# Kernel tuning notes

Hardware: AMD Instinct MI355X
Metric: run time of the kernel (lower is better)

## Reference

```python
import jax, jax.numpy as jnp
import numpy as np
import math

L, Bt, ED, H, LU = 1024, 64, 512, 512, 60
PSSM_DIM = 21

def setup_inputs() -> dict:
    key = jax.random.key(0)
    ks = jax.random.split(key, 16)
    seq = jax.random.randint(ks[0], (L, Bt), 0, 20)
    pssm = jax.random.uniform(ks[1], (L, Bt, PSSM_DIM), dtype=jnp.float32)
    length = jnp.full((Bt,), L, dtype=jnp.int32)  # all full-length -> packing is identity
    embed = jax.random.normal(ks[2], (20, ED), dtype=jnp.float32)
    s = 1.0 / math.sqrt(H)
    def u(k, shape):
        return jax.random.uniform(k, shape, minval=-s, maxval=s, dtype=jnp.float32)
    Wih_f = u(ks[3], (4 * H, ED + PSSM_DIM)); Whh_f = u(ks[4], (4 * H, H))
    bih_f = u(ks[5], (4 * H,)); bhh_f = u(ks[6], (4 * H,))
    Wih_b = u(ks[7], (4 * H, ED + PSSM_DIM)); Whh_b = u(ks[8], (4 * H, H))
    bih_b = u(ks[9], (4 * H,)); bhh_b = u(ks[10], (4 * H,))
    sl = 1.0 / math.sqrt(2 * H)
    W_lin = jax.random.uniform(ks[11], (LU, 2 * H), minval=-sl, maxval=sl, dtype=jnp.float32)
    b_lin = jax.random.uniform(ks[12], (LU,), minval=-sl, maxval=sl, dtype=jnp.float32)
    alphabet = jax.random.uniform(ks[13], (LU, 3), minval=-math.pi, maxval=math.pi, dtype=jnp.float32)
    return dict(seq=seq, pssm=pssm, length=length, embed=embed,
                Wih_f=Wih_f, Whh_f=Whh_f, bih_f=bih_f, bhh_f=bhh_f,
                Wih_b=Wih_b, Whh_b=Whh_b, bih_b=bih_b, bhh_b=bhh_b,
                W_lin=W_lin, b_lin=b_lin, alphabet=alphabet)

def _lstm_dir(x, Wih, Whh, bih, bhh, reverse):
    # x: [L, B, D] -> hidden states [L, B, H]
    b = bih + bhh
    xg = jnp.einsum('lbd,gd->lbg', x, Wih) + b  # precompute input gates
    B = x.shape[1]
    Hh = Whh.shape[1]
    def step(carry, xgt):
        h, c = carry
        z = xgt + h @ Whh.T
        i, f, g, o = jnp.split(z, 4, axis=-1)  # torch gate order i,f,g,o
        i = jax.nn.sigmoid(i); f = jax.nn.sigmoid(f)
        g = jnp.tanh(g); o = jax.nn.sigmoid(o)
        c = f * c + i * g
        h = o * jnp.tanh(c)
        return (h, c), h
    init = (jnp.zeros((B, Hh), x.dtype), jnp.zeros((B, Hh), x.dtype))
    _, hs = jax.lax.scan(step, init, xg, reverse=reverse)
    return hs

def _extend(A, B, C, R, T, P):
    # NeRF extension: A,B,C [Bt,3]; R,T scalars; P [Bt] torsion
    D2 = jnp.stack([-R * jnp.cos(T) * jnp.ones_like(P),
                    R * jnp.cos(P) * jnp.sin(T),
                    R * jnp.sin(P) * jnp.sin(T)], axis=1)  # [Bt,3]
    bc = C - B
    bc = bc / jnp.linalg.norm(bc, axis=1, keepdims=True)
    n = jnp.cross(B - A, bc)
    n = n / jnp.linalg.norm(n, axis=1, keepdims=True)
    M = jnp.stack([bc, jnp.cross(n, bc), n], axis=2)  # [Bt,3,3]
    return jnp.einsum('bij,bj->bi', M, D2) + C

def reference(seq, pssm, length, embed, Wih_f, Whh_f, bih_f, bhh_f,
              Wih_b, Whh_b, bih_b, bhh_b, W_lin, b_lin, alphabet):
    bond_lengths = jnp.array([132.868, 145.801, 152.326], dtype=pssm.dtype)
    bond_angles = jnp.array([2.028, 2.124, 1.941], dtype=pssm.dtype)
    x = jnp.concatenate([embed[seq], pssm], axis=2)  # [L,B,ED+21]
    h_f = _lstm_dir(x, Wih_f, Whh_f, bih_f, bhh_f, reverse=False)
    h_b = _lstm_dir(x, Wih_b, Whh_b, bih_b, bhh_b, reverse=True)
    lstm_out = jnp.concatenate([h_f, h_b], axis=2)  # [L,B,2H]
    logits = jnp.einsum('lbh,uh->lbu', lstm_out, W_lin) + b_lin
    p = jax.nn.softmax(logits, axis=2)  # [L,B,LU]
    sin = p @ jnp.sin(alphabet)  # [L,B,3]
    cos = p @ jnp.cos(alphabet)
    phi = jnp.arctan2(sin, cos)  # [L,B,3] torsion angles
    B_ = seq.shape[1]
    init_coords = jnp.broadcast_to(jnp.eye(3, dtype=pssm.dtype)[:, None, :], (3, B_, 3))
    def residue_step(carry, phi_i):
        A, Bp, C = carry
        outs = []
        for j in range(3):  # N, CA, C backbone atoms
            D = _extend(A, Bp, C, bond_lengths[j], bond_angles[j], phi_i[:, j])
            A, Bp, C = Bp, C, D
            outs.append(D)
        return (A, Bp, C), jnp.stack(outs)  # [3,Bt,3]
    carry0 = (init_coords[0], init_coords[1], init_coords[2])
    _, new = jax.lax.scan(residue_step, carry0, phi)  # [L,3,Bt,3]
    coords = jnp.concatenate([init_coords, new.reshape(-1, B_, 3)], axis=0)  # [3+3L,B,3]
    return coords
```

## Files before the change

### kernel.cpp

```cpp
#include <hip/hip_runtime.h>
#include <hip/hip_bf16.h>
#include <hip/hip_fp16.h>
#include <math.h>

constexpr int L    = 1024;
constexpr int B    = 64;
constexpr int H    = 512;
constexpr int ED   = 512;
constexpr int PSSM = 21;
constexpr int DIN  = ED + PSSM;
constexpr int LU   = 60;
constexpr int HB   = H * B;
constexpr int NWG_DIR = 32;
constexpr int UPW  = 16;

typedef __attribute__((ext_vector_type(8))) _Float16 half8;
typedef __attribute__((ext_vector_type(4))) float f32x4;

__global__ __launch_bounds__(256) void prep_e2(
    const float* __restrict__ Wih_f, const float* __restrict__ Wih_b,
    const float* __restrict__ bih_f, const float* __restrict__ bhh_f,
    const float* __restrict__ bih_b, const float* __restrict__ bhh_b,
    const float* __restrict__ embed, float* __restrict__ E2)
{
    int idx  = blockIdx.x * 256 + threadIdx.x;
    int col  = idx & 2047;
    int rest = idx >> 11;
    int s    = rest % 20;
    int dir  = rest / 20;
    const float* W  = dir ? Wih_b : Wih_f;
    const float* er = embed + (size_t)s * ED;
    const float* wr = W + (size_t)col * DIN;
    float a = 0.f;
    #pragma unroll 8
    for (int k = 0; k < ED; ++k) a = fmaf(er[k], wr[k], a);
    a += (dir ? bih_b : bih_f)[col] + (dir ? bhh_b : bhh_f)[col];
    E2[idx] = a;
}

__global__ __launch_bounds__(256) void prep_whh(
    const float* __restrict__ Whh_f, const float* __restrict__ Whh_b,
    unsigned short* __restrict__ hi, unsigned short* __restrict__ lo)
{
    int idx = blockIdx.x * 256 + threadIdx.x;
    const int NPD = 2048 * 512;
    float w = (idx < NPD) ? Whh_f[idx] : Whh_b[idx - NPD];
    __half h = __float2half_rn(w);
    __half l2 = __float2half_rn(w - __half2float(h));
    hi[idx] = __half_as_ushort(h);
    lo[idx] = __half_as_ushort(l2);
}

__global__ __launch_bounds__(256, 1) void lstm_mfma(
    const float* __restrict__ E2, const float* __restrict__ pssm,
    const int* __restrict__ seq,
    const float* __restrict__ Wih_f, const float* __restrict__ Wih_b,
    const unsigned short* __restrict__ WhhHi, const unsigned short* __restrict__ WhhLo,
    unsigned short* __restrict__ ring,
    unsigned short* __restrict__ hs16_f, unsigned short* __restrict__ hs16_b,
    int* __restrict__ cnt)
{
    __shared__ unsigned short bhi[4 * 16 * 64 * 8];
    __shared__ unsigned short blo[4 * 16 * 64 * 8];
    __shared__ float wpsh[4][PSSM][16];
    __shared__ float wesh[20][68];
    __shared__ unsigned short tbuf[4][16][20];

    const int wg    = blockIdx.x;
    const int dir   = wg >> 5;
    const int wslot = wg & 31;
    const int j0    = wslot * UPW;
    const int tid   = threadIdx.x;
    const int l     = tid & 63;
    const int q     = tid >> 6;
    const int u     = l & 15;
    const int kh    = l >> 4;
    const int m0    = q * 16 + kh * 4;

    const float* Wih = dir ? Wih_b : Wih_f;
    const float* E2d = E2 + (size_t)dir * 20 * 2048;
    const unsigned short* Whi = WhhHi + (size_t)dir * 2048 * 512;
    const unsigned short* Wlo = WhhLo + (size_t)dir * 2048 * 512;
    unsigned short* rbase = ring + (size_t)dir * 2 * HB;
    unsigned short* hist  = dir ? hs16_b : hs16_f;
    int* qflg = cnt + ((size_t)(dir * 4 + q)) * L;

    for (int i = tid; i < 4 * 16 * 64; i += 256) {
        int l2 = i & 63, c2 = (i >> 6) & 15, g2 = i >> 10;
        int row = g2 * 512 + j0 + (l2 & 15);
        size_t off = (size_t)row * 512 + c2 * 32 + (l2 >> 4) * 8;
        *(uint4*)&bhi[i * 8] = *(const uint4*)(Whi + off);
        *(uint4*)&blo[i * 8] = *(const uint4*)(Wlo + off);
    }
    for (int i = tid; i < 4 * PSSM * 16; i += 256) {
        int uu = i & 15, rem = i >> 4;
        int k = rem % PSSM, g = rem / PSSM;
        wpsh[g][k][uu] = Wih[(size_t)(g * 512 + j0 + uu) * DIN + ED + k];
    }
    for (int i = tid; i < 20 * 64; i += 256) {
        int sym = i >> 6, col = i & 63;
        wesh[sym][col] = E2d[(size_t)sym * 2048 + (col >> 4) * 512 + j0 + (col & 15)];
    }
    __syncthreads();

    float creg[4] = {0.f, 0.f, 0.f, 0.f};

    for (int s = 0; s < L; ++s) {
        const int t = dir ? (L - 1 - s) : s;

        float zin[4][4];
        int sb[4];
        #pragma unroll
        for (int r = 0; r < 4; ++r) sb[r] = seq[t * B + m0 + r];
        #pragma unroll
        for (int g = 0; g < 4; ++g)
            #pragma unroll
            for (int r = 0; r < 4; ++r)
                zin[g][r] = wesh[sb[r]][g * 16 + u];
        {
            const float* pb = pssm + (size_t)t * B * PSSM;
            #pragma unroll
            for (int k = 0; k < PSSM; ++k) {
                float p0 = pb[(m0 + 0) * PSSM + k];
                float p1 = pb[(m0 + 1) * PSSM + k];
                float p2 = pb[(m0 + 2) * PSSM + k];
                float p3 = pb[(m0 + 3) * PSSM + k];
                #pragma unroll
                for (int g = 0; g < 4; ++g) {
                    float wv = wpsh[g][k][u];
                    zin[g][0] = fmaf(p0, wv, zin[g][0]);
                    zin[g][1] = fmaf(p1, wv, zin[g][1]);
                    zin[g][2] = fmaf(p2, wv, zin[g][2]);
                    zin[g][3] = fmaf(p3, wv, zin[g][3]);
                }
            }
        }

        f32x4 acc[4];
        #pragma unroll
        for (int g = 0; g < 4; ++g)
            acc[g] = (f32x4){zin[g][0], zin[g][1], zin[g][2], zin[g][3]};

        if (s > 0) {
            {
                const int* fp = qflg + (s - 1);
                int it = 0;
                while (true) {
                    int v;
                    asm volatile("global_load_dword %0, %1, off sc0 sc1\n\t"
                                 "s_waitcnt vmcnt(0)"
                                 : "=v"(v) : "v"(fp) : "memory");
                    if (__all(v >= NWG_DIR)) break;
                    __builtin_amdgcn_s_sleep(1);
                    if (++it > (1 << 17)) break;
                }
            }
            uint4 af[16];
            const unsigned short* src =
                rbase + ((s + 1) & 1) * HB + (size_t)(q * 16 + u) * 512 + kh * 8;
            #pragma unroll
            for (int c = 0; c < 16; ++c)
                asm volatile("global_load_dwordx4 %0, %1, off sc0 sc1"
                             : "=&v"(af[c]) : "v"(src + c * 32) : "memory");
            asm volatile("s_waitcnt vmcnt(0)" ::: "memory");
            __builtin_amdgcn_sched_barrier(0);

            #pragma unroll
            for (int c = 0; c < 16; ++c) {
                half8 ah = *(const half8*)&af[c];
                #pragma unroll
                for (int g = 0; g < 4; ++g) {
                    half8 bh = *(const half8*)&bhi[((g * 16 + c) * 64 + l) * 8];
                    half8 bl = *(const half8*)&blo[((g * 16 + c) * 64 + l) * 8];
                    acc[g] = __builtin_amdgcn_mfma_f32_16x16x32_f16(ah, bh, acc[g], 0, 0, 0);
                    acc[g] = __builtin_amdgcn_mfma_f32_16x16x32_f16(ah, bl, acc[g], 0, 0, 0);
                }
            }
        }

        #pragma unroll
        for (int r = 0; r < 4; ++r) {
            float iv = acc[0][r], fv = acc[1][r], gv = acc[2][r], ov = acc[3][r];
            iv = 1.f / (1.f + __expf(-iv));
            fv = 1.f / (1.f + __expf(-fv));
            gv = tanhf(gv);
            ov = 1.f / (1.f + __expf(-ov));
            float cc = fv * creg[r] + iv * gv;
            creg[r] = cc;
            float hv = ov * tanhf(cc);
            tbuf[q][kh * 4 + r][u] = __half_as_ushort(__float2half_rn(hv));
        }

        {
            int bq = l >> 2, g4 = (l & 3) * 4;
            int bb = q * 16 + bq;
            unsigned v0 = *(const unsigned*)&tbuf[q][bq][g4];
            unsigned v1 = *(const unsigned*)&tbuf[q][bq][g4 + 2];
            unsigned short* d = rbase + (s & 1) * HB + bb * 512 + j0 + g4;
            asm volatile("global_store_dword %0, %1, off sc0 sc1"
                         :: "v"(d), "v"(v0) : "memory");
            asm volatile("global_store_dword %0, %1, off sc0 sc1"
                         :: "v"(d + 2), "v"(v1) : "memory");
            unsigned short* hd = hist + (size_t)t * HB + bb * 512 + j0 + g4;
            *(unsigned*)hd = v0;
            *(unsigned*)(hd + 2) = v1;
        }
        asm volatile("s_waitcnt vmcnt(0)" ::: "memory");
        if (l == 0) atomicAdd(qflg + s, 1);
    }
}

__global__ __launch_bounds__(256) void proj_softmax(
    const unsigned short* __restrict__ hsf, const unsigned short* __restrict__ hsb,
    const float* __restrict__ W_lin, const float* __restrict__ b_lin,
    const float* __restrict__ alphabet, float* __restrict__ sp, float* __restrict__ cp)
{
    const int t   = blockIdx.x;
    const int tid = threadIdx.x;
    const int b   = tid & 63;
    const int ug  = __builtin_amdgcn_readfirstlane(tid >> 6);
    constexpr int NU = 15;

    __shared__ float lg[B][LU];
    __shared__ float sa[LU][3], ca[LU][3];
    if (tid < LU) {
        for (int k = 0; k < 3; ++k) {
            float a = alphabet[tid * 3 + k];
            sa[tid][k] = __sinf(a);
            ca[tid][k] = __cosf(a);
        }
    }

    const int u0 = ug * NU;
    float acc[NU];
    #pragma unroll
    for (int i = 0; i < NU; ++i) acc[i] = b_lin[u0 + i];

    #pragma unroll
    for (int half = 0; half < 2; ++half) {
        const unsigned short* hp =
            (half ? hsb : hsf) + (size_t)t * HB + (size_t)b * H;
        for (int j8 = 0; j8 < H / 8; ++j8) {
            uint4 hv4 = *(const uint4*)(hp + j8 * 8);
            const __half* hx = (const __half*)&hv4;
            float hvv[8];
            #pragma unroll
            for (int jj = 0; jj < 8; ++jj) hvv[jj] = __half2float(hx[jj]);
            #pragma unroll
            for (int i = 0; i < NU; ++i) {
                const float* wr = W_lin + (size_t)(u0 + i) * (2 * H) + half * H + j8 * 8;
                float4 wa = *(const float4*)wr;
                float4 wb = *(const float4*)(wr + 4);
                acc[i] = fmaf(hvv[0], wa.x, acc[i]);
                acc[i] = fmaf(hvv[1], wa.y, acc[i]);
                acc[i] = fmaf(hvv[2], wa.z, acc[i]);
                acc[i] = fmaf(hvv[3], wa.w, acc[i]);
                acc[i] = fmaf(hvv[4], wb.x, acc[i]);
                acc[i] = fmaf(hvv[5], wb.y, acc[i]);
                acc[i] = fmaf(hvv[6], wb.z, acc[i]);
                acc[i] = fmaf(hvv[7], wb.w, acc[i]);
            }
        }
    }
    #pragma unroll
    for (int i = 0; i < NU; ++i) lg[b][u0 + i] = acc[i];
    __syncthreads();

    if (tid < B) {
        float m = -1e30f;
        for (int u = 0; u < LU; ++u) m = fmaxf(m, lg[tid][u]);
        float sv[3] = {0, 0, 0}, cv[3] = {0, 0, 0};
        for (int u = 0; u < LU; ++u) {
            float e = __expf(lg[tid][u] - m);
            for (int k = 0; k < 3; ++k) {
                sv[k] = fmaf(e, sa[u][k], sv[k]);
                cv[k] = fmaf(e, ca[u][k], cv[k]);
            }
        }
        for (int k = 0; k < 3; ++k) {
            float r = rsqrtf(sv[k] * sv[k] + cv[k] * cv[k]);
            sp[((size_t)t * B + tid) * 3 + k] = sv[k] * r;
            cp[((size_t)t * B + tid) * 3 + k] = cv[k] * r;
        }
    }
}

__global__ void geometry(const float* __restrict__ sp, const float* __restrict__ cp,
                         float* __restrict__ out)
{
    const int b = threadIdx.x;
    const float Rj[3] = {132.868f, 145.801f, 152.326f};
    const float Tj[3] = {2.028f, 2.124f, 1.941f};
    float cT[3], sT[3];
    for (int j = 0; j < 3; ++j) { cT[j] = cosf(Tj[j]); sT[j] = sinf(Tj[j]); }

    for (int r = 0; r < 3; ++r)
        for (int c = 0; c < 3; ++c)
            out[((size_t)r * B + b) * 3 + c] = (r == c) ? 1.f : 0.f;

    float Ax = 1.f, Ay = 0.f, Az = 0.f;
    float Bx = 0.f, By = 1.f, Bz = 0.f;
    float Cx = 0.f, Cy = 0.f, Cz = 1.f;

    for (int t = 0; t < L; ++t) {
        for (int j = 0; j < 3; ++j) {
            float sP = sp[((size_t)t * B + b) * 3 + j];
            float cP = cp[((size_t)t * B + b) * 3 + j];
            float d0 = -Rj[j] * cT[j];
            float d1 =  Rj[j] * cP * sT[j];
            float d2 =  Rj[j] * sP * sT[j];

            float bcx = Cx - Bx, bcy = Cy - By, bcz = Cz - Bz;
            float inv = rsqrtf(bcx * bcx + bcy * bcy + bcz * bcz);
            bcx *= inv; bcy *= inv; bcz *= inv;

            float abx = Bx - Ax, aby = By - Ay, abz = Bz - Az;
            float nx = aby * bcz - abz * bcy;
            float ny = abz * bcx - abx * bcz;
            float nz = abx * bcy - aby * bcx;
            inv = rsqrtf(nx * nx + ny * ny + nz * nz);
            nx *= inv; ny *= inv; nz *= inv;

            float mx = ny * bcz - nz * bcy;
            float my = nz * bcx - nx * bcz;
            float mz = nx * bcy - ny * bcx;

            float Dx = bcx * d0 + mx * d1 + nx * d2 + Cx;
            float Dy = bcy * d0 + my * d1 + ny * d2 + Cy;
            float Dz = bcz * d0 + mz * d1 + nz * d2 + Cz;

            size_t r = 3 + 3 * (size_t)t + j;
            out[(r * B + b) * 3 + 0] = Dx;
            out[(r * B + b) * 3 + 1] = Dy;
            out[(r * B + b) * 3 + 2] = Dz;

            Ax = Bx; Ay = By; Az = Bz;
            Bx = Cx; By = Cy; Bz = Cz;
            Cx = Dx; Cy = Dy; Cz = Dz;
        }
    }
}

extern "C" void kernel_launch(void* const* d_in, const int* in_sizes, int n_in,
                              void* d_out, int out_size, void* d_ws, size_t ws_size,
                              hipStream_t stream)
{
    const int*   seq      = (const int*)  d_in[0];
    const float* pssm     = (const float*)d_in[1];
    const float* embed    = (const float*)d_in[3];
    const float* Wih_f    = (const float*)d_in[4];
    const float* Whh_f    = (const float*)d_in[5];
    const float* bih_f    = (const float*)d_in[6];
    const float* bhh_f    = (const float*)d_in[7];
    const float* Wih_b    = (const float*)d_in[8];
    const float* Whh_b    = (const float*)d_in[9];
    const float* bih_b    = (const float*)d_in[10];
    const float* bhh_b    = (const float*)d_in[11];
    const float* W_lin    = (const float*)d_in[12];
    const float* b_lin    = (const float*)d_in[13];
    const float* alphabet = (const float*)d_in[14];
    float* out = (float*)d_out;

    char* ws = (char*)d_ws;
    unsigned short* ring = (unsigned short*)ws;
    int* cnt       = (int*)(ws + 262144);
    float* E2      = (float*)(ws + 294912);
    unsigned short* WhhHi = (unsigned short*)(ws + 622592);
    unsigned short* WhhLo = (unsigned short*)(ws + 622592 + 4194304);
    unsigned short* hs16_f = (unsigned short*)(ws + 622592 + 8388608);
    unsigned short* hs16_b = (unsigned short*)(ws + 622592 + 8388608 + 67108864);
    float* sp      = (float*)(ws + 294912);
    float* cp      = (float*)(ws + 294912 + 786432);

    (void)hipMemsetAsync(cnt, 0, 32768, stream);

    prep_e2<<<dim3(320), dim3(256), 0, stream>>>(Wih_f, Wih_b, bih_f, bhh_f,
                                                 bih_b, bhh_b, embed, E2);
    prep_whh<<<dim3(8192), dim3(256), 0, stream>>>(Whh_f, Whh_b, WhhHi, WhhLo);

    lstm_mfma<<<dim3(2 * NWG_DIR), dim3(256), 0, stream>>>(
        E2, pssm, seq, Wih_f, Wih_b, WhhHi, WhhLo,
        ring, hs16_f, hs16_b, cnt);

    proj_softmax<<<dim3(L), dim3(256), 0, stream>>>(
        hs16_f, hs16_b, W_lin, b_lin, alphabet, sp, cp);
    geometry<<<dim3(1), dim3(64), 0, stream>>>(sp, cp, out);
}
```

Measured before the change: 7.603 ms.

## Replace counter-flag barrier with sentinel-poisoned history buffer polling

```diff
diff --git a/kernel.cpp b/kernel.cpp
--- a/kernel.cpp
+++ b/kernel.cpp
@@ -56,9 +56,7 @@
     const int* __restrict__ seq,
     const float* __restrict__ Wih_f, const float* __restrict__ Wih_b,
     const unsigned short* __restrict__ WhhHi, const unsigned short* __restrict__ WhhLo,
-    unsigned short* __restrict__ ring,
-    unsigned short* __restrict__ hs16_f, unsigned short* __restrict__ hs16_b,
-    int* __restrict__ cnt)
+    unsigned short* __restrict__ hs16_f, unsigned short* __restrict__ hs16_b)
 {
     __shared__ unsigned short bhi[4 * 16 * 64 * 8];
     __shared__ unsigned short blo[4 * 16 * 64 * 8];
@@ -81,9 +79,7 @@
     const float* E2d = E2 + (size_t)dir * 20 * 2048;
     const unsigned short* Whi = WhhHi + (size_t)dir * 2048 * 512;
     const unsigned short* Wlo = WhhLo + (size_t)dir * 2048 * 512;
-    unsigned short* rbase = ring + (size_t)dir * 2 * HB;
     unsigned short* hist  = dir ? hs16_b : hs16_f;
-    int* qflg = cnt + ((size_t)(dir * 4 + q)) * L;
 
     for (int i = tid; i < 4 * 16 * 64; i += 256) {
         int l2 = i & 63, c2 = (i >> 6) & 15, g2 = i >> 10;
@@ -106,7 +102,8 @@
     float creg[4] = {0.f, 0.f, 0.f, 0.f};
 
     for (int s = 0; s < L; ++s) {
-        const int t = dir ? (L - 1 - s) : s;
+        const int t     = dir ? (L - 1 - s) : s;
+        const int tprev = dir ? (t + 1) : (t - 1);
 
         float zin[4][4];
         int sb[4];
@@ -142,27 +139,29 @@
             acc[g] = (f32x4){zin[g][0], zin[g][1], zin[g][2], zin[g][3]};
 
         if (s > 0) {
-            {
-                const int* fp = qflg + (s - 1);
-                int it = 0;
-                while (true) {
-                    int v;
-                    asm volatile("global_load_dword %0, %1, off sc0 sc1\n\t"
-                                 "s_waitcnt vmcnt(0)"
-                                 : "=v"(v) : "v"(fp) : "memory");
-                    if (__all(v >= NWG_DIR)) break;
-                    __builtin_amdgcn_s_sleep(1);
-                    if (++it > (1 << 17)) break;
-                }
-            }
             uint4 af[16];
             const unsigned short* src =
-                rbase + ((s + 1) & 1) * HB + (size_t)(q * 16 + u) * 512 + kh * 8;
-            #pragma unroll
-            for (int c = 0; c < 16; ++c)
-                asm volatile("global_load_dwordx4 %0, %1, off sc0 sc1"
-                             : "=&v"(af[c]) : "v"(src + c * 32) : "memory");
-            asm volatile("s_waitcnt vmcnt(0)" ::: "memory");
+                hist + (size_t)tprev * HB + (size_t)(q * 16 + u) * 512 + kh * 8;
+            int it = 0;
+            while (true) {
+                #pragma unroll
+                for (int c = 0; c < 16; ++c)
+                    asm volatile("global_load_dwordx4 %0, %1, off sc0 sc1"
+                                 : "=&v"(af[c]) : "v"(src + c * 32) : "memory");
+                asm volatile("s_waitcnt vmcnt(0)" ::: "memory");
+                __builtin_amdgcn_sched_barrier(0);
+                unsigned bad = 0u;
+                #pragma unroll
+                for (int c = 0; c < 16; ++c) {
+                    bad |= (unsigned)(af[c].x == 0xFFFFFFFFu);
+                    bad |= (unsigned)(af[c].y == 0xFFFFFFFFu);
+                    bad |= (unsigned)(af[c].z == 0xFFFFFFFFu);
+                    bad |= (unsigned)(af[c].w == 0xFFFFFFFFu);
+                }
+                if (__all(bad == 0u)) break;
+                __builtin_amdgcn_s_sleep(1);
+                if (++it > (1 << 17)) break;
+            }
             __builtin_amdgcn_sched_barrier(0);
 
             #pragma unroll
@@ -196,17 +195,12 @@
             int bb = q * 16 + bq;
             unsigned v0 = *(const unsigned*)&tbuf[q][bq][g4];
             unsigned v1 = *(const unsigned*)&tbuf[q][bq][g4 + 2];
-            unsigned short* d = rbase + (s & 1) * HB + bb * 512 + j0 + g4;
+            unsigned short* hd = hist + (size_t)t * HB + bb * 512 + j0 + g4;
             asm volatile("global_store_dword %0, %1, off sc0 sc1"
-                         :: "v"(d), "v"(v0) : "memory");
+                         :: "v"(hd), "v"(v0) : "memory");
             asm volatile("global_store_dword %0, %1, off sc0 sc1"
-                         :: "v"(d + 2), "v"(v1) : "memory");
-            unsigned short* hd = hist + (size_t)t * HB + bb * 512 + j0 + g4;
-            *(unsigned*)hd = v0;
-            *(unsigned*)(hd + 2) = v1;
-        }
-        asm volatile("s_waitcnt vmcnt(0)" ::: "memory");
-        if (l == 0) atomicAdd(qflg + s, 1);
+                         :: "v"(hd + 2), "v"(v1) : "memory");
+        }
     }
 }
 
@@ -362,25 +356,22 @@
     float* out = (float*)d_out;
 
     char* ws = (char*)d_ws;
-    unsigned short* ring = (unsigned short*)ws;
-    int* cnt       = (int*)(ws + 262144);
-    float* E2      = (float*)(ws + 294912);
-    unsigned short* WhhHi = (unsigned short*)(ws + 622592);
-    unsigned short* WhhLo = (unsigned short*)(ws + 622592 + 4194304);
-    unsigned short* hs16_f = (unsigned short*)(ws + 622592 + 8388608);
-    unsigned short* hs16_b = (unsigned short*)(ws + 622592 + 8388608 + 67108864);
-    float* sp      = (float*)(ws + 294912);
-    float* cp      = (float*)(ws + 294912 + 786432);
-
-    (void)hipMemsetAsync(cnt, 0, 32768, stream);
+    unsigned short* hs16_f = (unsigned short*)ws;
+    unsigned short* hs16_b = (unsigned short*)(ws + 67108864);
+    float* E2      = (float*)(ws + 134217728);
+    unsigned short* WhhHi = (unsigned short*)(ws + 134545408);
+    unsigned short* WhhLo = (unsigned short*)(ws + 138739712);
+    float* sp      = (float*)(ws + 134217728);
+    float* cp      = (float*)(ws + 134217728 + 786432);
+
+    (void)hipMemsetAsync(ws, 0xFF, 134217728, stream);
 
     prep_e2<<<dim3(320), dim3(256), 0, stream>>>(Wih_f, Wih_b, bih_f, bhh_f,
                                                  bih_b, bhh_b, embed, E2);
     prep_whh<<<dim3(8192), dim3(256), 0, stream>>>(Whh_f, Whh_b, WhhHi, WhhLo);
 
     lstm_mfma<<<dim3(2 * NWG_DIR), dim3(256), 0, stream>>>(
-        E2, pssm, seq, Wih_f, Wih_b, WhhHi, WhhLo,
-        ring, hs16_f, hs16_b, cnt);
+        E2, pssm, seq, Wih_f, Wih_b, WhhHi, WhhLo, hs16_f, hs16_b);
 
     proj_softmax<<<dim3(L), dim3(256), 0, stream>>>(
         hs16_f, hs16_b, W_lin, b_lin, alphabet, sp, cp);
```

Measured after the change: 7.378 ms. -3.0%, faster.
